# Kernel optimization log

Hardware: AMD Instinct MI355X
Metric: run time of the kernel (lower is better)

## Reference

```python
import jax, jax.numpy as jnp
import numpy as np
from jax import lax

N = 4194304
DELTA_T = 1.0
ETA = 1.0
QN = 1.5 * 3600.0
INITIAL_X2 = 1.0


def setup_inputs() -> dict:
    key = jax.random.key(0)
    k1, k2, k3 = jax.random.split(key, 3)
    return {
        "uk_sequence": jax.random.normal(k1, (N,), dtype=jnp.float32),
        "Rp": jnp.float32(1.0),
        "Cp": jnp.float32(1.0),
        "R0": jax.random.uniform(k2, (), dtype=jnp.float32),
        "a_coeffs": jax.random.normal(k3, (9,), dtype=jnp.float32) * 0.1,
    }


def _forward(uk_sequence, Rp, Cp, R0, a_coeffs):
    # Diagonal linear SSM, state = (x1, x2)
    A00 = jnp.exp(-DELTA_T / (Rp * Cp))            # decay of RC branch
    B0 = Rp * (1.0 - A00)                           # input gain on x1
    B1 = jnp.float32(-ETA * DELTA_T / QN)           # constant coulomb-counting gain

    def step(carry, u):
        x1, x2 = carry
        nxt = (A00 * x1 + B0 * u, x2 + B1 * u)
        return nxt, carry                           # emit state BEFORE update (xk[k])

    init = (jnp.float32(0.0), jnp.float32(INITIAL_X2))
    _, (x1s, x2s) = lax.scan(step, init, uk_sequence)  # each [N]

    # poly8(x2) = a0 + a1*x2 + ... + a8*x2^8 via Horner (highest-first for polyval)
    poly = jnp.polyval(a_coeffs[::-1], x2s)
    y = poly - x1s - R0 * uk_sequence               # [N]
    return y[:, None]                               # [N, 1] to match torch output


def reference(uk_sequence, Rp, Cp, R0, a_coeffs):
    return _forward(uk_sequence, Rp, Cp, R0, a_coeffs)
```

## Files before the change

kernel.cpp:

```cpp
#include <hip/hip_runtime.h>


constexpr int BLOCK = 256;
constexpr int TPER  = 8;
constexpr int CHUNK = BLOCK * TPER;
constexpr int NTOT  = 4194304;
constexpr int NB    = NTOT / CHUNK;
constexpr int APT   = NB / BLOCK;

__global__ __launch_bounds__(BLOCK) void kA_agg(
    const float* __restrict__ u,
    const float* __restrict__ Rp_p, const float* __restrict__ Cp_p,
    double* __restrict__ aggW, double* __restrict__ aggP)
{
    __shared__ double sW[BLOCK];
    __shared__ double sP[BLOCK];
    const int b = blockIdx.x, t = threadIdx.x;
    const double invRC = 1.0 / ((double)Rp_p[0] * (double)Cp_p[0]);
    const double A00   = exp(-invRC);

    const float4* up = (const float4*)(u + (size_t)b * CHUNK + (size_t)t * TPER);
    float4 v[2];
    v[0] = up[0]; v[1] = up[1];
    const float* uu = (const float*)v;

    double s = 0.0, p = 0.0;
#pragma unroll
    for (int i = 0; i < TPER; ++i) { s = A00 * s + (double)uu[i]; p += (double)uu[i]; }
    sW[t] = s; sP[t] = p;
    __syncthreads();

    double f = exp(-(double)TPER * invRC);
    for (int stride = 1; stride < BLOCK; stride <<= 1) {
        if ((t & (2 * stride - 1)) == 0) {
            sW[t] = sW[t] * f + sW[t + stride];
            sP[t] = sP[t] + sP[t + stride];
        }
        f *= f;
        __syncthreads();
    }
    if (t == 0) { aggW[b] = sW[0]; aggP[b] = sP[0]; }
}

__global__ __launch_bounds__(BLOCK) void kB_emit(
    const float* __restrict__ u,
    const float* __restrict__ Rp_p, const float* __restrict__ Cp_p,
    const float* __restrict__ R0_p, const float* __restrict__ ac,
    const double* __restrict__ aggW, const double* __restrict__ aggP,
    float* __restrict__ out)
{
    __shared__ double sS[2][BLOCK];
    __shared__ double sP[2][BLOCK];
    __shared__ double sRed[BLOCK / 64];
    __shared__ double sCW;

    const int b = blockIdx.x, t = threadIdx.x;
    const double Rp    = (double)Rp_p[0], Cp = (double)Cp_p[0];
    const double invRC = 1.0 / (Rp * Cp);
    const double A00   = exp(-invRC);
    const double B0    = Rp * (1.0 - A00);
    const double B1    = -1.0 / 5400.0;
    const double R0    = (double)R0_p[0];
    const double dC    = exp(-(double)CHUNK * invRC);

    const size_t base = (size_t)b * CHUNK + (size_t)t * TPER;
    const float4* up = (const float4*)(u + base);
    float4 v[2];
    v[0] = up[0]; v[1] = up[1];
    const float* uu = (const float*)v;

    double pc = 0.0;
#pragma unroll
    for (int i = 0; i < APT; ++i) {
        const int j = t * APT + i;
        if (j < b) pc += aggP[j];
    }
    for (int off = 32; off; off >>= 1) pc += __shfl_down(pc, off, 64);
    if ((t & 63) == 0) sRed[t >> 6] = pc;

    if (t == 0) {
        double cW;
        if (dC == 0.0) {
            cW = (b > 0) ? aggW[b - 1] : 0.0;
        } else {
            cW = 0.0;
            for (int j = 0; j < b; ++j) cW = cW * dC + aggW[j];
        }
        sCW = cW;
    }

    double s = 0.0, p = 0.0;
#pragma unroll
    for (int i = 0; i < TPER; ++i) { s = A00 * s + (double)uu[i]; p += (double)uu[i]; }
    sS[0][t] = s; sP[0][t] = p;
    __syncthreads();

    double carryP = 0.0;
#pragma unroll
    for (int w = 0; w < BLOCK / 64; ++w) carryP += sRed[w];
    const double carryW = sCW;

    double f = exp(-(double)TPER * invRC);
    int cur = 0;
    for (int d = 1; d < BLOCK; d <<= 1) {
        const int nxt = cur ^ 1;
        double w = sS[cur][t], q = sP[cur][t];
        if (t >= d) { w = sS[cur][t - d] * f + w; q = sP[cur][t - d] + q; }
        sS[nxt][t] = w; sP[nxt][t] = q;
        cur = nxt; f *= f;
        __syncthreads();
    }
    const double exW = t ? sS[cur][t - 1] : 0.0;
    const double exP = t ? sP[cur][t - 1] : 0.0;

    double a[9];
#pragma unroll
    for (int i = 0; i < 9; ++i) a[i] = (double)ac[i];

    double Wcur = carryW * exp(-(double)(TPER * t) * invRC) + exW;
    double Pcur = carryP + exP;

    float4 o[2];
    float* oy = (float*)o;
#pragma unroll
    for (int i = 0; i < TPER; ++i) {
        const double x2 = 1.0 + B1 * Pcur;
        double poly = a[8];
#pragma unroll
        for (int j = 7; j >= 0; --j) poly = poly * x2 + a[j];
        oy[i] = (float)(poly - B0 * Wcur - R0 * (double)uu[i]);
        Wcur = A00 * Wcur + (double)uu[i];
        Pcur += (double)uu[i];
    }
    float4* op = (float4*)(out + base);
    op[0] = o[0]; op[1] = o[1];
}

extern "C" void kernel_launch(void* const* d_in, const int* in_sizes, int n_in,
                              void* d_out, int out_size, void* d_ws, size_t ws_size,
                              hipStream_t stream) {
    const float* u    = (const float*)d_in[0];
    const float* Rp_p = (const float*)d_in[1];
    const float* Cp_p = (const float*)d_in[2];
    const float* R0_p = (const float*)d_in[3];
    const float* ac   = (const float*)d_in[4];
    float* out = (float*)d_out;

    double* wsW = (double*)d_ws;
    double* wsP = (double*)d_ws + NB;

    kA_agg <<<NB, BLOCK, 0, stream>>>(u, Rp_p, Cp_p, wsW, wsP);
    kB_emit<<<NB, BLOCK, 0, stream>>>(u, Rp_p, Cp_p, R0_p, ac, wsW, wsP, out);
}
```

Measured before the change: 87.50 us.

## Use wavefront shuffle scans, 16 elements per thread, and fp32 polynomial

Replaces the shared-memory tree reduction and Hillis-Steele scan with 64-lane shuffle-up scans plus a small cross-wave combine in shared memory, which removes most __syncthreads barriers. Doubles elements per thread to 16, halving the block count and the serial carry chain length in the emit kernel. Computes decay powers by repeated squaring instead of exp and evaluates the degree-8 polynomial in fp32 FMA instead of fp64. The fp32 polynomial and squaring-based powers may slightly change numerical accuracy.

```diff
diff --git a/kernel.cpp b/kernel.cpp
--- a/kernel.cpp
+++ b/kernel.cpp
@@ -2,10 +2,11 @@
 
 
 constexpr int BLOCK = 256;
-constexpr int TPER  = 8;
+constexpr int TPER  = 16;
 constexpr int CHUNK = BLOCK * TPER;
 constexpr int NTOT  = 4194304;
 constexpr int NB    = NTOT / CHUNK;
+constexpr int WPB   = BLOCK / 64;
 constexpr int APT   = NB / BLOCK;
 
 __global__ __launch_bounds__(BLOCK) void kA_agg(
@@ -13,33 +14,42 @@
     const float* __restrict__ Rp_p, const float* __restrict__ Cp_p,
     double* __restrict__ aggW, double* __restrict__ aggP)
 {
-    __shared__ double sW[BLOCK];
-    __shared__ double sP[BLOCK];
+    __shared__ double LW[WPB], LP[WPB];
     const int b = blockIdx.x, t = threadIdx.x;
+    const int lane = t & 63, w = t >> 6;
+
     const double invRC = 1.0 / ((double)Rp_p[0] * (double)Cp_p[0]);
-    const double A00   = exp(-invRC);
+    const double A00 = exp(-invRC);
+    const double a2 = A00 * A00, a4 = a2 * a2, a8 = a4 * a4;
+    const double f16 = a8 * a8;
 
     const float4* up = (const float4*)(u + (size_t)b * CHUNK + (size_t)t * TPER);
-    float4 v[2];
-    v[0] = up[0]; v[1] = up[1];
+    float4 v[4];
+    v[0] = up[0]; v[1] = up[1]; v[2] = up[2]; v[3] = up[3];
     const float* uu = (const float*)v;
 
     double s = 0.0, p = 0.0;
 #pragma unroll
     for (int i = 0; i < TPER; ++i) { s = A00 * s + (double)uu[i]; p += (double)uu[i]; }
-    sW[t] = s; sP[t] = p;
+
+    double fk = f16;
+#pragma unroll
+    for (int k = 1; k < 64; k <<= 1) {
+        const double sw = __shfl_up(s, k, 64);
+        const double pw = __shfl_up(p, k, 64);
+        if (lane >= k) { s = sw * fk + s; p += pw; }
+        fk *= fk;
+    }
+    if (lane == 63) { LW[w] = s; LP[w] = p; }
     __syncthreads();
 
-    double f = exp(-(double)TPER * invRC);
-    for (int stride = 1; stride < BLOCK; stride <<= 1) {
-        if ((t & (2 * stride - 1)) == 0) {
-            sW[t] = sW[t] * f + sW[t + stride];
-            sP[t] = sP[t] + sP[t + stride];
-        }
-        f *= f;
-        __syncthreads();
+    if (t == 0) {
+        double f1024 = f16;
+        for (int i = 0; i < 6; ++i) f1024 *= f1024;
+        double W = LW[0], P = LP[0];
+        for (int v2 = 1; v2 < WPB; ++v2) { W = W * f1024 + LW[v2]; P += LP[v2]; }
+        aggW[b] = W; aggP[b] = P;
     }
-    if (t == 0) { aggW[b] = sW[0]; aggP[b] = sP[0]; }
 }
 
 __global__ __launch_bounds__(BLOCK) void kB_emit(
@@ -49,24 +59,28 @@
     const double* __restrict__ aggW, const double* __restrict__ aggP,
     float* __restrict__ out)
 {
-    __shared__ double sS[2][BLOCK];
-    __shared__ double sP[2][BLOCK];
-    __shared__ double sRed[BLOCK / 64];
+    __shared__ double LW[WPB], LP[WPB];
+    __shared__ double sRed[WPB];
     __shared__ double sCW;
 
     const int b = blockIdx.x, t = threadIdx.x;
-    const double Rp    = (double)Rp_p[0], Cp = (double)Cp_p[0];
-    const double invRC = 1.0 / (Rp * Cp);
-    const double A00   = exp(-invRC);
-    const double B0    = Rp * (1.0 - A00);
-    const double B1    = -1.0 / 5400.0;
-    const double R0    = (double)R0_p[0];
-    const double dC    = exp(-(double)CHUNK * invRC);
+    const int lane = t & 63, w = t >> 6;
+
+    const double invRC = 1.0 / ((double)Rp_p[0] * (double)Cp_p[0]);
+    const double A00 = exp(-invRC);
+    const double B0  = (double)Rp_p[0] * (1.0 - A00);
+    const double B1  = -1.0 / 5400.0;
+    const float  R0f = R0_p[0];
+    const double a2 = A00 * A00, a4 = a2 * a2, a8 = a4 * a4;
+    const double f16 = a8 * a8;
+    double f1024 = f16;
+    for (int i = 0; i < 6; ++i) f1024 *= f1024;
+    const double dC = (f1024 * f1024) * (f1024 * f1024);
 
     const size_t base = (size_t)b * CHUNK + (size_t)t * TPER;
     const float4* up = (const float4*)(u + base);
-    float4 v[2];
-    v[0] = up[0]; v[1] = up[1];
+    float4 v[4];
+    v[0] = up[0]; v[1] = up[1]; v[2] = up[2]; v[3] = up[3];
     const float* uu = (const float*)v;
 
     double pc = 0.0;
@@ -75,8 +89,9 @@
         const int j = t * APT + i;
         if (j < b) pc += aggP[j];
     }
+#pragma unroll
     for (int off = 32; off; off >>= 1) pc += __shfl_down(pc, off, 64);
-    if ((t & 63) == 0) sRed[t >> 6] = pc;
+    if (lane == 0) sRed[w] = pc;
 
     if (t == 0) {
         double cW;
@@ -92,48 +107,54 @@
     double s = 0.0, p = 0.0;
 #pragma unroll
     for (int i = 0; i < TPER; ++i) { s = A00 * s + (double)uu[i]; p += (double)uu[i]; }
-    sS[0][t] = s; sP[0][t] = p;
+    double fk = f16;
+#pragma unroll
+    for (int k = 1; k < 64; k <<= 1) {
+        const double sw = __shfl_up(s, k, 64);
+        const double pw = __shfl_up(p, k, 64);
+        if (lane >= k) { s = sw * fk + s; p += pw; }
+        fk *= fk;
+    }
+    if (lane == 63) { LW[w] = s; LP[w] = p; }
     __syncthreads();
 
-    double carryP = 0.0;
+    double carryP_blk = 0.0;
 #pragma unroll
-    for (int w = 0; w < BLOCK / 64; ++w) carryP += sRed[w];
-    const double carryW = sCW;
+    for (int v2 = 0; v2 < WPB; ++v2) carryP_blk += sRed[v2];
 
-    double f = exp(-(double)TPER * invRC);
-    int cur = 0;
-    for (int d = 1; d < BLOCK; d <<= 1) {
-        const int nxt = cur ^ 1;
-        double w = sS[cur][t], q = sP[cur][t];
-        if (t >= d) { w = sS[cur][t - d] * f + w; q = sP[cur][t - d] + q; }
-        sS[nxt][t] = w; sP[nxt][t] = q;
-        cur = nxt; f *= f;
-        __syncthreads();
-    }
-    const double exW = t ? sS[cur][t - 1] : 0.0;
-    const double exP = t ? sP[cur][t - 1] : 0.0;
+    double cw = 0.0, cp = 0.0;
+    for (int v2 = 0; v2 < w; ++v2) { cw = cw * f1024 + LW[v2]; cp += LP[v2]; }
 
-    double a[9];
+    double fw = 1.0;
+    for (int v2 = 0; v2 < w; ++v2) fw *= f1024;
+
+    double fl = 1.0, bse = f16;
 #pragma unroll
-    for (int i = 0; i < 9; ++i) a[i] = (double)ac[i];
+    for (int k = 0; k < 6; ++k) { if (lane & (1 << k)) fl *= bse; bse *= bse; }
 
-    double Wcur = carryW * exp(-(double)(TPER * t) * invRC) + exW;
-    double Pcur = carryP + exP;
+    const double upW = __shfl_up(s, 1, 64);
+    const double upP = __shfl_up(p, 1, 64);
+    double Wcur = (lane ? upW : 0.0) + (cw + sCW * fw) * fl;
+    double Pcur = (lane ? upP : 0.0) + cp + carryP_blk;
 
-    float4 o[2];
+    float af[9];
+#pragma unroll
+    for (int i = 0; i < 9; ++i) af[i] = ac[i];
+
+    float4 o[4];
     float* oy = (float*)o;
 #pragma unroll
     for (int i = 0; i < TPER; ++i) {
-        const double x2 = 1.0 + B1 * Pcur;
-        double poly = a[8];
+        const float x2 = (float)(1.0 + B1 * Pcur);
+        float poly = af[8];
 #pragma unroll
-        for (int j = 7; j >= 0; --j) poly = poly * x2 + a[j];
-        oy[i] = (float)(poly - B0 * Wcur - R0 * (double)uu[i]);
+        for (int j = 7; j >= 0; --j) poly = fmaf(poly, x2, af[j]);
+        oy[i] = poly - (float)(B0 * Wcur) - R0f * uu[i];
         Wcur = A00 * Wcur + (double)uu[i];
         Pcur += (double)uu[i];
     }
     float4* op = (float4*)(out + base);
-    op[0] = o[0]; op[1] = o[1];
+    op[0] = o[0]; op[1] = o[1]; op[2] = o[2]; op[3] = o[3];
 }
 
 extern "C" void kernel_launch(void* const* d_in, const int* in_sizes, int n_in,
```

Result: faster. 85.17 us (-2.7%).
